# Performance work log

Hardware: AMD Instinct MI355X
Metric: run time of the kernel (lower is better)

The kernel has to match this reference:

```python
import jax, jax.numpy as jnp
import numpy as np

B, L, H, W, C = 2, 5, 48, 48, 256
M, D = 8, 32               # heads, dim_head; M*D == C
NT, NR = 2, 4              # num_types, num_relations
SCALE = D ** -0.5
EPS = 1e-5


def _xavier(k, shape):
    fan_out, fan_in = shape[-2], shape[-1]
    lim = (6.0 / (fan_in + fan_out)) ** 0.5
    return jax.random.uniform(k, shape, jnp.float32, -lim, lim)


def setup_inputs() -> dict:
    key = jax.random.key(0)
    ks = jax.random.split(key, 10)
    inner = M * D
    x = jax.random.normal(ks[0], (B, L, H, W, C), jnp.float32)
    mask = jnp.ones((B, H, W, L, L), jnp.int32)
    pe = jax.random.randint(ks[1], (B, L, H, W, 3), 0, NT).astype(jnp.float32)
    return dict(
        x=x, mask=mask, prior_encoding=pe,
        ln_w=jnp.ones((C,), jnp.float32), ln_b=jnp.zeros((C,), jnp.float32),
        q_weight=_xavier(ks[2], (NT, inner, C)), q_bias=jnp.zeros((NT, inner), jnp.float32),
        k_weight=_xavier(ks[3], (NT, inner, C)), k_bias=jnp.zeros((NT, inner), jnp.float32),
        v_weight=_xavier(ks[4], (NT, inner, C)), v_bias=jnp.zeros((NT, inner), jnp.float32),
        a_weight=_xavier(ks[5], (NT, C, inner)), a_bias=jnp.zeros((NT, C), jnp.float32),
        relation_att=_xavier(ks[6], (NR, M, D, D)),
        relation_msg=_xavier(ks[7], (NR, M, D, D)),
    )


def reference(x, mask, prior_encoding, ln_w, ln_b,
              q_weight, q_bias, k_weight, k_bias, v_weight, v_bias,
              a_weight, a_bias, relation_att, relation_msg):
    # PreNorm (torch LayerNorm: biased variance, eps=1e-5)
    mu = jnp.mean(x, axis=-1, keepdims=True)
    var = jnp.mean((x - mu) ** 2, axis=-1, keepdims=True)
    xn = (x - mu) * jax.lax.rsqrt(var + EPS) * ln_w + ln_b

    types = prior_encoding[:, :, 0, 0, 2].astype(jnp.int32)  # (B, L)
    xp = jnp.transpose(xn, (0, 2, 3, 1, 4))                  # (B, H, W, L, C)

    def type_linear(inp, wgt, b):
        # gather per-node-type weights (B,L,out,in) and project
        return (jnp.einsum('bhwlc,bloc->bhwlo', inp, wgt[types])
                + b[types][:, None, None, :, :])

    def to_heads(t):
        # (B,H,W,L,M*D) -> (B,M,H,W,L,D)
        return jnp.transpose(t.reshape(B, H, W, L, M, D), (0, 4, 1, 2, 3, 5))

    q = to_heads(type_linear(xp, q_weight, q_bias))
    k = to_heads(type_linear(xp, k_weight, k_bias))
    v = to_heads(type_linear(xp, v_weight, v_bias))

    # per-edge relation weights: rel_idx = t_i * num_types + t_j
    rel = types[:, :, None] * NT + types[:, None, :]          # (B, L, L)
    w_att = jnp.transpose(relation_att[rel], (0, 3, 1, 2, 4, 5))  # (B,M,L,L,D,D)
    w_msg = jnp.transpose(relation_msg[rel], (0, 3, 1, 2, 4, 5))  # (B,M,L,L,D,D)

    q_w = jnp.einsum('bmhwip,bmijpq->bmhwijq', q, w_att)
    att = jnp.einsum('bmhwijq,bmhwjq->bmhwij', q_w, k) * SCALE
    att = jnp.where(mask[:, None] == 0, -1e9, att)
    att = jax.nn.softmax(att, axis=-1)

    v_msg = jnp.einsum('bmijpc,bmhwjp->bmhwijc', w_msg, v)
    out = jnp.einsum('bmhwij,bmhwijc->bmhwic', att, v_msg)
    out = jnp.transpose(out, (0, 2, 3, 4, 1, 5)).reshape(B, H, W, L, C)

    # output projection with per-type weights (dropout = identity at eval)
    out = (jnp.einsum('bhwli,blci->bhwlc', out, a_weight[types])
           + a_bias[types][:, None, None, :, :])
    return jnp.transpose(out, (0, 3, 1, 2, 4))  # (B, L, H, W, C)
```

## Files before the change

kernel.cpp:

```cpp
#include <hip/hip_runtime.h>
#include <hip/hip_bf16.h>

#define BB 2
#define LL 5
#define HH 48
#define WW 48
#define CC 256
#define MM 8
#define DD 32
#define HWW (HH*WW)
#define NTOK (BB*LL*HWW)
#define INNER 256
#define NOUT 1280
#define SCALE_ATT 0.17677669529663687f

typedef __hip_bfloat16 bf16;
typedef short short8 __attribute__((ext_vector_type(8)));
typedef float f32x4  __attribute__((ext_vector_type(4)));

__device__ __forceinline__ float b2f(bf16 v){ return __bfloat162float(v); }
__device__ __forceinline__ bf16 f2b(float v){ return __float2bfloat16(v); }
__device__ __forceinline__ short f2s(float v){
  bf16 h = __float2bfloat16(v);
  return *reinterpret_cast<short*>(&h);
}

__global__ __launch_bounds__(256) void ln_stats_kernel(
    const float* __restrict__ x, float* __restrict__ mu, float* __restrict__ rstd)
{
  int tok  = blockIdx.x*4 + (threadIdx.x>>6);
  int lane = threadIdx.x & 63;
  const float4* xr = (const float4*)(x + (size_t)tok*CC);
  float4 v = xr[lane];
  float s  = v.x + v.y + v.z + v.w;
  float sq = v.x*v.x + v.y*v.y + v.z*v.z + v.w*v.w;
  #pragma unroll
  for(int off=32; off>=1; off>>=1){
    s  += __shfl_xor(s,  off, 64);
    sq += __shfl_xor(sq, off, 64);
  }
  if(lane==0){
    float m   = s  * (1.f/CC);
    float var = sq * (1.f/CC) - m*m;
    mu[tok]   = m;
    rstd[tok] = rsqrtf(var + 1e-5f);
  }
}

__global__ __launch_bounds__(256) void wcomp_kernel(
    const float* __restrict__ qw, const float* __restrict__ qb,
    const float* __restrict__ kw, const float* __restrict__ kb,
    const float* __restrict__ vw, const float* __restrict__ vb,
    const float* __restrict__ ra, const float* __restrict__ rm,
    bf16* __restrict__ W_all, float* __restrict__ b_all)
{
  int bid = blockIdx.x;
  int t = bid / 320, nb = bid % 320;
  int tid = threadIdx.x;
  int wv = tid>>6, lane = tid&63;
  int n = nb*4 + wv;

  float a0=0.f,a1=0.f,a2=0.f,a3=0.f, bias=0.f;
  if(n < 512 || n >= 768){
    bool isq = (n < 512);
    int nr = isq ? n : n-768;
    int s = nr>>8, mdp = nr&255, m = mdp>>5, dp = mdp&31;
    int r = isq ? (2*t+s) : (2*s+t);
    const float* rel  = (isq ? ra : rm) + ((size_t)r*MM + m)*DD*DD + dp;
    const float* wrow = (isq ? qw : vw) + (size_t)t*INNER*CC + (size_t)m*DD*CC;
    const float* brow = (isq ? qb : vb) + t*INNER + m*DD;
    #pragma unroll
    for(int p=0;p<DD;p++){
      float rv = rel[p*DD];
      float4 w4 = *(const float4*)(wrow + p*CC + lane*4);
      a0 += w4.x*rv; a1 += w4.y*rv; a2 += w4.z*rv; a3 += w4.w*rv;
      bias += brow[p]*rv;
    }
  } else {
    int o = n - 512;
    float4 w4 = *(const float4*)(kw + (size_t)t*INNER*CC + (size_t)o*CC + lane*4);
    a0=w4.x; a1=w4.y; a2=w4.z; a3=w4.w;
    bias = kb[t*INNER + o];
  }
  bf16* dst = W_all + ((size_t)t*NOUT + n)*CC + lane*4;
  dst[0]=f2b(a0); dst[1]=f2b(a1); dst[2]=f2b(a2); dst[3]=f2b(a3);
  if(lane==0) b_all[t*NOUT + n] = bias;
}

__global__ __launch_bounds__(256) void qkvm_gemm_kernel(
    const float* __restrict__ x,  const float* __restrict__ pe,
    const float* __restrict__ mu, const float* __restrict__ rstd,
    const float* __restrict__ lnw, const float* __restrict__ lnb,
    const bf16* __restrict__ W_all, const float* __restrict__ b_all,
    bf16* __restrict__ qkvm)
{
  int g = blockIdx.z;
  int t = (int)pe[(size_t)g*HWW*3 + 2];
  int o_base = blockIdx.x * 128;
  const bf16*  wsel = W_all + ((size_t)t*NOUT + o_base)*CC;
  const float* bsel = b_all + t*NOUT;
  int row_base = blockIdx.y*128;
  int tid = threadIdx.x;
  int tokbase = g*HWW + row_base;

  __shared__ __align__(16) short A_s[128*64];
  __shared__ __align__(16) short B_s[128*64];

  int wv = tid>>6, lane = tid&63;
  int wr = wv>>1, wc = wv&1;
  int l16 = lane&15, l4 = lane>>4;
  int kc = tid & 7;
  int rsub = tid >> 3;

  f32x4 acc[4][4];
  #pragma unroll
  for(int i=0;i<4;i++)
    #pragma unroll
    for(int j=0;j<4;j++) acc[i][j] = (f32x4){0.f,0.f,0.f,0.f};

  for(int kk=0; kk<CC; kk+=64){
    if(kk) __syncthreads();
    float4 w0 = *(const float4*)(lnw + kk + kc*8);
    float4 w1 = *(const float4*)(lnw + kk + kc*8 + 4);
    float4 c0 = *(const float4*)(lnb + kk + kc*8);
    float4 c1 = *(const float4*)(lnb + kk + kc*8 + 4);
    #pragma unroll
    for(int tt=0; tt<4; tt++){
      int row = rsub + tt*32;
      int tok = tokbase + row;
      float m = mu[tok], rs = rstd[tok];
      const float4* src = (const float4*)(x + (size_t)tok*CC + kk + kc*8);
      float4 xa = src[0], xb = src[1];
      short8 pk;
      pk[0]=f2s((xa.x-m)*rs*w0.x+c0.x); pk[1]=f2s((xa.y-m)*rs*w0.y+c0.y);
      pk[2]=f2s((xa.z-m)*rs*w0.z+c0.z); pk[3]=f2s((xa.w-m)*rs*w0.w+c0.w);
      pk[4]=f2s((xb.x-m)*rs*w1.x+c1.x); pk[5]=f2s((xb.y-m)*rs*w1.y+c1.y);
      pk[6]=f2s((xb.z-m)*rs*w1.z+c1.z); pk[7]=f2s((xb.w-m)*rs*w1.w+c1.w);
      int el = (row*64 + kc*8) ^ ((row&7)<<3);
      *reinterpret_cast<short8*>(&A_s[el]) = pk;
    }
    #pragma unroll
    for(int tt=0; tt<4; tt++){
      int n = rsub + tt*32;
      short8 pk = *reinterpret_cast<const short8*>(wsel + (size_t)n*CC + kk + kc*8);
      int el = (n*64 + kc*8) ^ ((n&7)<<3);
      *reinterpret_cast<short8*>(&B_s[el]) = pk;
    }
    __syncthreads();
    #pragma unroll
    for(int ks=0; ks<2; ks++){
      short8 af[4], bfr[4];
      #pragma unroll
      for(int fr=0; fr<4; fr++){
        int row = wr*64 + fr*16 + l16;
        int el = (row*64 + ks*32 + l4*8) ^ ((row&7)<<3);
        af[fr] = *reinterpret_cast<const short8*>(&A_s[el]);
      }
      #pragma unroll
      for(int fc=0; fc<4; fc++){
        int n = wc*64 + fc*16 + l16;
        int el = (n*64 + ks*32 + l4*8) ^ ((n&7)<<3);
        bfr[fc] = *reinterpret_cast<const short8*>(&B_s[el]);
      }
      #pragma unroll
      for(int fr=0; fr<4; fr++)
        #pragma unroll
        for(int fc=0; fc<4; fc++)
          acc[fr][fc] = __builtin_amdgcn_mfma_f32_16x16x32_bf16(af[fr], bfr[fc], acc[fr][fc], 0,0,0);
    }
  }
  #pragma unroll
  for(int fr=0; fr<4; fr++){
    #pragma unroll
    for(int fc=0; fc<4; fc++){
      int ocol = o_base + wc*64 + fc*16 + l16;
      float bias = bsel[ocol];
      #pragma unroll
      for(int r=0; r<4; r++){
        int row = row_base + wr*64 + fr*16 + l4*4 + r;
        qkvm[((size_t)g*HWW + row)*NOUT + ocol] = f2b(acc[fr][fc][r] + bias);
      }
    }
  }
}

__global__ __launch_bounds__(256) void attn_lite_kernel(
    const bf16* __restrict__ qkvm, const float* __restrict__ pe,
    const int*  __restrict__ mask, bf16* __restrict__ attn_out)
{
  int pix = blockIdx.x;
  int b = pix / HWW, hw = pix - b*HWW;
  int tid = threadIdx.x;
  int m = tid>>5, d = tid&31;

  __shared__ int st[LL];
  __shared__ unsigned mbS;
  if(tid==0) mbS = 0u;
  if(tid<LL) st[tid] = (int)pe[(size_t)(b*LL+tid)*HWW*3 + 2];
  __syncthreads();
  const int* mrow = mask + ((size_t)b*HWW + hw)*25;
  if(tid<25 && mrow[tid]==0) atomicOr(&mbS, 1u<<tid);
  __syncthreads();
  unsigned mb = mbS;

  float qa[LL][2], kv[LL], vm[LL][2];
  #pragma unroll
  for(int l=0;l<LL;l++){
    size_t base = ((size_t)(b*LL+l)*HWW + hw)*NOUT + m*DD + d;
    qa[l][0] = b2f(qkvm[base]);
    qa[l][1] = b2f(qkvm[base+256]);
    kv[l]    = b2f(qkvm[base+512]);
    vm[l][0] = b2f(qkvm[base+768]);
    vm[l][1] = b2f(qkvm[base+1024]);
  }

  float p[LL][LL];
  #pragma unroll
  for(int i=0;i<LL;i++){
    #pragma unroll
    for(int j=0;j<LL;j++){
      int stj = st[j];
      float part = (stj ? qa[i][1] : qa[i][0]) * kv[j];
      #pragma unroll
      for(int off=16; off>=1; off>>=1) part += __shfl_xor(part, off, 32);
      p[i][j] = (mb & (1u<<(i*5+j))) ? -1e9f : part*SCALE_ATT;
    }
  }
  #pragma unroll
  for(int i=0;i<LL;i++){
    float mx = p[i][0];
    #pragma unroll
    for(int j=1;j<LL;j++) mx = fmaxf(mx, p[i][j]);
    float ssum = 0.f;
    #pragma unroll
    for(int j=0;j<LL;j++){ p[i][j] = __expf(p[i][j]-mx); ssum += p[i][j]; }
    float inv = 1.f/ssum;
    int sti = st[i];
    float o = 0.f;
    #pragma unroll
    for(int j=0;j<LL;j++) o += p[i][j] * (sti ? vm[j][1] : vm[j][0]);
    o *= inv;
    attn_out[(((size_t)b*HWW + hw)*LL + i)*CC + m*DD + d] = f2b(o);
  }
}

__global__ __launch_bounds__(256) void out_gemm_kernel(
    const bf16* __restrict__ attn_out, const float* __restrict__ pe,
    const float* __restrict__ aw, const float* __restrict__ ab,
    float* __restrict__ out)
{
  int g = blockIdx.z; int b = g/LL, l = g%LL;
  int t = (int)pe[(size_t)g*HWW*3 + 2];
  int o_base = blockIdx.x*128;
  int row_base = blockIdx.y*128;
  int tid = threadIdx.x;
  const float* wsel = aw + ((size_t)t*CC + o_base)*CC;

  __shared__ __align__(16) short A_s[128*64];
  __shared__ __align__(16) short B_s[128*64];

  int wv = tid>>6, lane = tid&63;
  int wr = wv>>1, wc = wv&1;
  int l16 = lane&15, l4 = lane>>4;
  int kc = tid & 7;
  int rsub = tid >> 3;

  f32x4 acc[4][4];
  #pragma unroll
  for(int i=0;i<4;i++)
    #pragma unroll
    for(int j=0;j<4;j++) acc[i][j] = (f32x4){0.f,0.f,0.f,0.f};

  for(int kk=0; kk<CC; kk+=64){
    if(kk) __syncthreads();
    #pragma unroll
    for(int tt=0; tt<4; tt++){
      int row = rsub + tt*32;
      short8 pk = *reinterpret_cast<const short8*>(
          attn_out + (((size_t)(b*HWW) + row_base + row)*LL + l)*CC + kk + kc*8);
      int el = (row*64 + kc*8) ^ ((row&7)<<3);
      *reinterpret_cast<short8*>(&A_s[el]) = pk;
    }
    #pragma unroll
    for(int tt=0; tt<4; tt++){
      int n = rsub + tt*32;
      const float4* src = (const float4*)(wsel + (size_t)n*CC + kk + kc*8);
      float4 ba = src[0], bb = src[1];
      short8 pk;
      pk[0]=f2s(ba.x); pk[1]=f2s(ba.y); pk[2]=f2s(ba.z); pk[3]=f2s(ba.w);
      pk[4]=f2s(bb.x); pk[5]=f2s(bb.y); pk[6]=f2s(bb.z); pk[7]=f2s(bb.w);
      int el = (n*64 + kc*8) ^ ((n&7)<<3);
      *reinterpret_cast<short8*>(&B_s[el]) = pk;
    }
    __syncthreads();
    #pragma unroll
    for(int ks=0; ks<2; ks++){
      short8 af[4], bfr[4];
      #pragma unroll
      for(int fr=0; fr<4; fr++){
        int row = wr*64 + fr*16 + l16;
        int el = (row*64 + ks*32 + l4*8) ^ ((row&7)<<3);
        af[fr] = *reinterpret_cast<const short8*>(&A_s[el]);
      }
      #pragma unroll
      for(int fc=0; fc<4; fc++){
        int n = wc*64 + fc*16 + l16;
        int el = (n*64 + ks*32 + l4*8) ^ ((n&7)<<3);
        bfr[fc] = *reinterpret_cast<const short8*>(&B_s[el]);
      }
      #pragma unroll
      for(int fr=0; fr<4; fr++)
        #pragma unroll
        for(int fc=0; fc<4; fc++)
          acc[fr][fc] = __builtin_amdgcn_mfma_f32_16x16x32_bf16(af[fr], bfr[fc], acc[fr][fc], 0,0,0);
    }
  }
  #pragma unroll
  for(int fr=0; fr<4; fr++){
    #pragma unroll
    for(int fc=0; fc<4; fc++){
      int ocol = o_base + wc*64 + fc*16 + l16;
      float bias = ab[t*CC + ocol];
      #pragma unroll
      for(int r=0; r<4; r++){
        int row = row_base + wr*64 + fr*16 + l4*4 + r;
        out[((size_t)g*HWW + row)*CC + ocol] = acc[fr][fc][r] + bias;
      }
    }
  }
}

extern "C" void kernel_launch(void* const* d_in, const int* in_sizes, int n_in,
                              void* d_out, int out_size, void* d_ws, size_t ws_size,
                              hipStream_t stream)
{
  const float* x   = (const float*)d_in[0];
  const int*   mask= (const int*)  d_in[1];
  const float* pe  = (const float*)d_in[2];
  const float* lnw = (const float*)d_in[3];
  const float* lnb = (const float*)d_in[4];
  const float* qw  = (const float*)d_in[5];
  const float* qb  = (const float*)d_in[6];
  const float* kw  = (const float*)d_in[7];
  const float* kb  = (const float*)d_in[8];
  const float* vw  = (const float*)d_in[9];
  const float* vb  = (const float*)d_in[10];
  const float* aw  = (const float*)d_in[11];
  const float* ab  = (const float*)d_in[12];
  const float* ra  = (const float*)d_in[13];
  const float* rm  = (const float*)d_in[14];

  char* ws = (char*)d_ws;
  float* mu    = (float*)ws;
  float* rstd  = (float*)(ws + 92160);
  bf16*  W_all = (bf16*) (ws + 184320);
  float* b_all = (float*)(ws + 1495040);
  bf16*  qkvm  = (bf16*) (ws + 1505280);
  bf16*  attn  = (bf16*) (ws + 60487680);
  float* out   = (float*)d_out;

  hipLaunchKernelGGL(ln_stats_kernel, dim3(NTOK/4), dim3(256), 0, stream, x, mu, rstd);
  hipLaunchKernelGGL(wcomp_kernel, dim3(640), dim3(256), 0, stream,
                     qw, qb, kw, kb, vw, vb, ra, rm, W_all, b_all);
  hipLaunchKernelGGL(qkvm_gemm_kernel, dim3(10, 18, 10), dim3(256), 0, stream,
                     x, pe, mu, rstd, lnw, lnb, W_all, b_all, qkvm);
  hipLaunchKernelGGL(attn_lite_kernel, dim3(BB*HWW), dim3(256), 0, stream,
                     qkvm, pe, mask, attn);
  hipLaunchKernelGGL(out_gemm_kernel, dim3(2, 18, 10), dim3(256), 0, stream,
                     attn, pe, aw, ab, out);
}
```

Measured before the change: 209.8 us.

## Widen QKVM GEMM N-tile to 256 and stage attention I/O through LDS

The QKVM GEMM now computes 256 output columns per block instead of 128, so the LayerNorm-applied A tile is built once per 256 columns rather than twice. This halves the redundant x reads and normalization work but doubles accumulator registers and B-tile LDS, which may lower occupancy. The attention kernel now loads each pixel's 5x1280 qkvm row into LDS with 16-byte vector loads instead of scattered 2-byte global loads. It also stages its outputs in LDS so they can be written back with vectorized stores.

```diff
diff --git a/kernel.cpp b/kernel.cpp
--- a/kernel.cpp
+++ b/kernel.cpp
@@ -24,6 +24,9 @@
   bf16 h = __float2bfloat16(v);
   return *reinterpret_cast<short*>(&h);
 }
+__device__ __forceinline__ float s2f(short s){
+  return __uint_as_float(((unsigned)(unsigned short)s)<<16);
+}
 
 __global__ __launch_bounds__(256) void ln_stats_kernel(
     const float* __restrict__ x, float* __restrict__ mu, float* __restrict__ rstd)
@@ -96,7 +99,7 @@
 {
   int g = blockIdx.z;
   int t = (int)pe[(size_t)g*HWW*3 + 2];
-  int o_base = blockIdx.x * 128;
+  int o_base = blockIdx.x * 256;
   const bf16*  wsel = W_all + ((size_t)t*NOUT + o_base)*CC;
   const float* bsel = b_all + t*NOUT;
   int row_base = blockIdx.y*128;
@@ -104,7 +107,7 @@
   int tokbase = g*HWW + row_base;
 
   __shared__ __align__(16) short A_s[128*64];
-  __shared__ __align__(16) short B_s[128*64];
+  __shared__ __align__(16) short B_s[256*64];
 
   int wv = tid>>6, lane = tid&63;
   int wr = wv>>1, wc = wv&1;
@@ -112,11 +115,13 @@
   int kc = tid & 7;
   int rsub = tid >> 3;
 
-  f32x4 acc[4][4];
-  #pragma unroll
-  for(int i=0;i<4;i++)
-    #pragma unroll
-    for(int j=0;j<4;j++) acc[i][j] = (f32x4){0.f,0.f,0.f,0.f};
+  f32x4 acc[2][4][4];
+  #pragma unroll
+  for(int c=0;c<2;c++)
+    #pragma unroll
+    for(int i=0;i<4;i++)
+      #pragma unroll
+      for(int j=0;j<4;j++) acc[c][i][j] = (f32x4){0.f,0.f,0.f,0.f};
 
   for(int kk=0; kk<CC; kk+=64){
     if(kk) __syncthreads();
@@ -140,7 +145,7 @@
       *reinterpret_cast<short8*>(&A_s[el]) = pk;
     }
     #pragma unroll
-    for(int tt=0; tt<4; tt++){
+    for(int tt=0; tt<8; tt++){
       int n = rsub + tt*32;
       short8 pk = *reinterpret_cast<const short8*>(wsel + (size_t)n*CC + kk + kc*8);
       int el = (n*64 + kc*8) ^ ((n&7)<<3);
@@ -149,7 +154,7 @@
     __syncthreads();
     #pragma unroll
     for(int ks=0; ks<2; ks++){
-      short8 af[4], bfr[4];
+      short8 af[4];
       #pragma unroll
       for(int fr=0; fr<4; fr++){
         int row = wr*64 + fr*16 + l16;
@@ -157,28 +162,35 @@
         af[fr] = *reinterpret_cast<const short8*>(&A_s[el]);
       }
       #pragma unroll
+      for(int ct=0; ct<2; ct++){
+        short8 bfr[4];
+        #pragma unroll
+        for(int fc=0; fc<4; fc++){
+          int n = ct*128 + wc*64 + fc*16 + l16;
+          int el = (n*64 + ks*32 + l4*8) ^ ((n&7)<<3);
+          bfr[fc] = *reinterpret_cast<const short8*>(&B_s[el]);
+        }
+        #pragma unroll
+        for(int fr=0; fr<4; fr++)
+          #pragma unroll
+          for(int fc=0; fc<4; fc++)
+            acc[ct][fr][fc] = __builtin_amdgcn_mfma_f32_16x16x32_bf16(af[fr], bfr[fc], acc[ct][fr][fc], 0,0,0);
+      }
+    }
+  }
+  #pragma unroll
+  for(int ct=0; ct<2; ct++){
+    #pragma unroll
+    for(int fr=0; fr<4; fr++){
+      #pragma unroll
       for(int fc=0; fc<4; fc++){
-        int n = wc*64 + fc*16 + l16;
-        int el = (n*64 + ks*32 + l4*8) ^ ((n&7)<<3);
-        bfr[fc] = *reinterpret_cast<const short8*>(&B_s[el]);
-      }
-      #pragma unroll
-      for(int fr=0; fr<4; fr++)
+        int ocol = o_base + ct*128 + wc*64 + fc*16 + l16;
+        float bias = bsel[ocol];
         #pragma unroll
-        for(int fc=0; fc<4; fc++)
-          acc[fr][fc] = __builtin_amdgcn_mfma_f32_16x16x32_bf16(af[fr], bfr[fc], acc[fr][fc], 0,0,0);
-    }
-  }
-  #pragma unroll
-  for(int fr=0; fr<4; fr++){
-    #pragma unroll
-    for(int fc=0; fc<4; fc++){
-      int ocol = o_base + wc*64 + fc*16 + l16;
-      float bias = bsel[ocol];
-      #pragma unroll
-      for(int r=0; r<4; r++){
-        int row = row_base + wr*64 + fr*16 + l4*4 + r;
-        qkvm[((size_t)g*HWW + row)*NOUT + ocol] = f2b(acc[fr][fc][r] + bias);
+        for(int r=0; r<4; r++){
+          int row = row_base + wr*64 + fr*16 + l4*4 + r;
+          qkvm[((size_t)g*HWW + row)*NOUT + ocol] = f2b(acc[ct][fr][fc][r] + bias);
+        }
       }
     }
   }
@@ -193,11 +205,20 @@
   int tid = threadIdx.x;
   int m = tid>>5, d = tid&31;
 
+  __shared__ __align__(16) short lds16[LL*NOUT];
   __shared__ int st[LL];
   __shared__ unsigned mbS;
   if(tid==0) mbS = 0u;
   if(tid<LL) st[tid] = (int)pe[(size_t)(b*LL+tid)*HWW*3 + 2];
-  __syncthreads();
+  #pragma unroll
+  for(int i=0;i<4;i++){
+    int idx = tid + i*256;
+    if(idx < 800){
+      int l = idx/160, c = idx - l*160;
+      *reinterpret_cast<short8*>(&lds16[l*NOUT + c*8]) =
+        *reinterpret_cast<const short8*>(qkvm + ((size_t)(b*LL+l)*HWW + hw)*NOUT + c*8);
+    }
+  }
   const int* mrow = mask + ((size_t)b*HWW + hw)*25;
   if(tid<25 && mrow[tid]==0) atomicOr(&mbS, 1u<<tid);
   __syncthreads();
@@ -206,12 +227,12 @@
   float qa[LL][2], kv[LL], vm[LL][2];
   #pragma unroll
   for(int l=0;l<LL;l++){
-    size_t base = ((size_t)(b*LL+l)*HWW + hw)*NOUT + m*DD + d;
-    qa[l][0] = b2f(qkvm[base]);
-    qa[l][1] = b2f(qkvm[base+256]);
-    kv[l]    = b2f(qkvm[base+512]);
-    vm[l][0] = b2f(qkvm[base+768]);
-    vm[l][1] = b2f(qkvm[base+1024]);
+    int base = l*NOUT + m*DD + d;
+    qa[l][0] = s2f(lds16[base]);
+    qa[l][1] = s2f(lds16[base+256]);
+    kv[l]    = s2f(lds16[base+512]);
+    vm[l][0] = s2f(lds16[base+768]);
+    vm[l][1] = s2f(lds16[base+1024]);
   }
 
   float p[LL][LL];
@@ -226,6 +247,7 @@
       p[i][j] = (mb & (1u<<(i*5+j))) ? -1e9f : part*SCALE_ATT;
     }
   }
+  float oreg[LL];
   #pragma unroll
   for(int i=0;i<LL;i++){
     float mx = p[i][0];
@@ -239,8 +261,16 @@
     float o = 0.f;
     #pragma unroll
     for(int j=0;j<LL;j++) o += p[i][j] * (sti ? vm[j][1] : vm[j][0]);
-    o *= inv;
-    attn_out[(((size_t)b*HWW + hw)*LL + i)*CC + m*DD + d] = f2b(o);
+    oreg[i] = o * inv;
+  }
+  __syncthreads();
+  #pragma unroll
+  for(int i=0;i<LL;i++) lds16[i*CC + m*DD + d] = f2s(oreg[i]);
+  __syncthreads();
+  if(tid < 160){
+    int l = tid >> 5, c = tid & 31;
+    *reinterpret_cast<short8*>(attn_out + (((size_t)b*HWW + hw)*LL + l)*CC + c*8) =
+      *reinterpret_cast<const short8*>(&lds16[l*CC + c*8]);
   }
 }
 
@@ -362,7 +392,7 @@
   hipLaunchKernelGGL(ln_stats_kernel, dim3(NTOK/4), dim3(256), 0, stream, x, mu, rstd);
   hipLaunchKernelGGL(wcomp_kernel, dim3(640), dim3(256), 0, stream,
                      qw, qb, kw, kb, vw, vb, ra, rm, W_all, b_all);
-  hipLaunchKernelGGL(qkvm_gemm_kernel, dim3(10, 18, 10), dim3(256), 0, stream,
+  hipLaunchKernelGGL(qkvm_gemm_kernel, dim3(5, 18, 10), dim3(256), 0, stream,
                      x, pe, mu, rstd, lnw, lnb, W_all, b_all, qkvm);
   hipLaunchKernelGGL(attn_lite_kernel, dim3(BB*HWW), dim3(256), 0, stream,
                      qkvm, pe, mask, attn);
```

Result: slower. 239.7 us (+14.3%).
